# Optimization experiments

Measured on AMD Instinct MI355X. Metric: run time of the kernel, lower is better.

Reference implementation:

```python
import jax, jax.numpy as jnp
import numpy as np

B, S, D = 4, 4096, 1024

def setup_inputs() -> dict:
    key = jax.random.key(0)
    ks = jax.random.split(key, 7)
    scale = 1.0 / np.sqrt(D)
    X  = jax.random.normal(ks[0], (B, S, D), dtype=jnp.float32)
    Wq = jax.random.normal(ks[1], (D, D), dtype=jnp.float32) * scale
    bq = jnp.zeros((D,), dtype=jnp.float32)
    Wk = jax.random.normal(ks[2], (D, D), dtype=jnp.float32) * scale
    bk = jnp.zeros((D,), dtype=jnp.float32)
    Wv = jax.random.normal(ks[3], (D, D), dtype=jnp.float32) * scale
    bv = jnp.zeros((D,), dtype=jnp.float32)
    return {"X": X, "Wq": Wq, "bq": bq, "Wk": Wk, "bk": bk, "Wv": Wv, "bv": bv}

def reference(X, Wq, bq, Wk, bk, Wv, bv):
    # Linear projections (torch Linear: x @ W.T + b; here W stored as [D_in, D_out])
    Q = jnp.einsum('bsd,de->bse', X, Wq) + bq
    K = jnp.einsum('bsd,de->bse', X, Wk) + bk
    V = jnp.einsum('bsd,de->bse', X, Wv) + bv
    inv_sqrt_d = 1.0 / jnp.sqrt(jnp.float32(X.shape[-1]))
    scores = jnp.einsum('bqd,bkd->bqk', Q, K) * inv_sqrt_d  # [B,S,S]
    weights = jax.nn.sigmoid(scores)  # elementwise, no row normalization
    return jnp.einsum('bqk,bkd->bqd', weights, V)
```

## Files before the change

### kernel.cpp

```cpp
#include <hip/hip_runtime.h>
#include <hip/hip_bf16.h>

typedef __bf16 bf16_t;
typedef bf16_t bf16x8 __attribute__((ext_vector_type(8)));
typedef float f32x4 __attribute__((ext_vector_type(4)));

constexpr int BM = 128, BN = 128, BK = 32;
constexpr int D_DIM = 1024;
constexpr int S_DIM = 4096;
constexpr int B_DIM = 4;

__global__ void cast_f32_bf16(const float* __restrict__ in, bf16_t* __restrict__ out) {
  size_t i = ((size_t)blockIdx.x * blockDim.x + threadIdx.x) * 8;
  float4 a = *(const float4*)(in + i);
  float4 b = *(const float4*)(in + i + 4);
  bf16x8 o;
  o[0] = (bf16_t)a.x; o[1] = (bf16_t)a.y; o[2] = (bf16_t)a.z; o[3] = (bf16_t)a.w;
  o[4] = (bf16_t)b.x; o[5] = (bf16_t)b.y; o[6] = (bf16_t)b.z; o[7] = (bf16_t)b.w;
  *(bf16x8*)(out + i) = o;
}

__global__ void transpose_cast_1024(const float* __restrict__ in, bf16_t* __restrict__ out) {
  __shared__ float t[32][33];
  int x0 = blockIdx.x * 32, y0 = blockIdx.y * 32;
#pragma unroll
  for (int i = 0; i < 32; i += 8)
    t[threadIdx.y + i][threadIdx.x] =
        in[(size_t)(y0 + threadIdx.y + i) * D_DIM + (x0 + threadIdx.x)];
  __syncthreads();
#pragma unroll
  for (int i = 0; i < 32; i += 8)
    out[(size_t)(x0 + threadIdx.y + i) * D_DIM + (y0 + threadIdx.x)] =
        (bf16_t)t[threadIdx.x][threadIdx.y + i];
}

__device__ __forceinline__ void stage128x32(const bf16_t* __restrict__ g, int ld,
                                            bf16_t* lds, int tid) {
  int w = tid >> 6;
  int r = tid >> 2;
  int c = (tid & 3) * 8;
  const bf16_t* g0 = g + (size_t)r * ld + c;
  const bf16_t* g1 = g0 + (size_t)64 * ld;
  bf16_t* l0 = lds + w * 512;
  __builtin_amdgcn_global_load_lds((const __attribute__((address_space(1))) void*)g0,
                                   (__attribute__((address_space(3))) void*)l0, 16, 0, 0);
  __builtin_amdgcn_global_load_lds((const __attribute__((address_space(1))) void*)g1,
                                   (__attribute__((address_space(3))) void*)(l0 + 2048), 16, 0, 0);
}

template <int EPI, bool SWAP>
__global__ __launch_bounds__(256) void gemm_bt(
    const bf16_t* __restrict__ A, const bf16_t* __restrict__ Bt,
    void* __restrict__ C0, void* __restrict__ C1, void* __restrict__ C2,
    const float* __restrict__ b0, const float* __restrict__ b1, const float* __restrict__ b2,
    int K, int lda, int ldb, int ldc, float scale,
    size_t sA, size_t sB, size_t sC) {
  __shared__ bf16_t As[2 * BM * BK];
  __shared__ bf16_t Bs[2 * BN * BK];
  const int tid = threadIdx.x;
  const int lane = tid & 63;
  const int w = tid >> 6;
  const int wr = (w >> 1) * 64;
  const int wc = (w & 1) * 64;
  const int fm = lane & 15;
  const int fko = (lane >> 4) * 8;

  const int bx = SWAP ? blockIdx.y : blockIdx.x;
  const int by = SWAP ? blockIdx.x : blockIdx.y;

  const bf16_t* Ag = A + (size_t)blockIdx.z * sA + (size_t)by * BM * lda;
  const bf16_t* Bg = Bt + (size_t)blockIdx.z * sB + (size_t)bx * BN * ldb;

  f32x4 acc[4][4] = {};

  for (int k0 = 0; k0 < K; k0 += 2 * BK) {
    stage128x32(Ag + k0, lda, As, tid);
    stage128x32(Ag + k0 + BK, lda, As + BM * BK, tid);
    stage128x32(Bg + k0, ldb, Bs, tid);
    stage128x32(Bg + k0 + BK, ldb, Bs + BN * BK, tid);
    __syncthreads();
#pragma unroll
    for (int h = 0; h < 2; ++h) {
      const bf16_t* as = As + h * BM * BK;
      const bf16_t* bs = Bs + h * BN * BK;
      bf16x8 af[4], bfr[4];
#pragma unroll
      for (int i = 0; i < 4; ++i)
        af[i] = *(const bf16x8*)&as[(wr + i * 16 + fm) * BK + fko];
#pragma unroll
      for (int j = 0; j < 4; ++j)
        bfr[j] = *(const bf16x8*)&bs[(wc + j * 16 + fm) * BK + fko];
#pragma unroll
      for (int i = 0; i < 4; ++i)
#pragma unroll
        for (int j = 0; j < 4; ++j)
          acc[i][j] = __builtin_amdgcn_mfma_f32_16x16x32_bf16(af[i], bfr[j], acc[i][j], 0, 0, 0);
    }
    __syncthreads();
  }

  const int row0 = by * BM + wr + (lane >> 4) * 4;
  const int col0 = bx * BN + wc + fm;

  if constexpr (EPI == 0) {
    const int seg = (bx * BN) >> 10;
    const float* bias = (seg == 0) ? b0 : (seg == 1) ? b1 : b2;
#pragma unroll
    for (int i = 0; i < 4; ++i) {
#pragma unroll
      for (int j = 0; j < 4; ++j) {
        const int n = col0 + j * 16;
        const int nl = n & 1023;
        const float bv = bias[nl];
#pragma unroll
        for (int r = 0; r < 4; ++r) {
          const int m = row0 + i * 16 + r;
          float v = acc[i][j][r] + bv;
          if (seg < 2) {
            bf16_t* C = (bf16_t*)(seg == 0 ? C0 : C1);
            C[(size_t)m * D_DIM + nl] = (bf16_t)v;
          } else {
            bf16_t* C = (bf16_t*)C2;
            C[((size_t)(m >> 12) << 22) + (size_t)nl * S_DIM + (m & (S_DIM - 1))] = (bf16_t)v;
          }
        }
      }
    }
  } else {
#pragma unroll
    for (int i = 0; i < 4; ++i) {
#pragma unroll
      for (int j = 0; j < 4; ++j) {
        const int n = col0 + j * 16;
#pragma unroll
        for (int r = 0; r < 4; ++r) {
          const int m = row0 + i * 16 + r;
          float v = acc[i][j][r];
          if constexpr (EPI == 2) {
            bf16_t* C = (bf16_t*)C0 + (size_t)blockIdx.z * sC;
            float s = 1.0f / (1.0f + __expf(-v * scale));
            C[(size_t)m * ldc + n] = (bf16_t)s;
          } else {
            float* C = (float*)C0 + (size_t)blockIdx.z * sC;
            C[(size_t)m * ldc + n] = v;
          }
        }
      }
    }
  }
}

extern "C" void kernel_launch(void* const* d_in, const int* in_sizes, int n_in,
                              void* d_out, int out_size, void* d_ws, size_t ws_size,
                              hipStream_t stream) {
  const float* X  = (const float*)d_in[0];
  const float* Wq = (const float*)d_in[1];
  const float* bq = (const float*)d_in[2];
  const float* Wk = (const float*)d_in[3];
  const float* bk = (const float*)d_in[4];
  const float* Wv = (const float*)d_in[5];
  const float* bv = (const float*)d_in[6];
  float* out = (float*)d_out;

  const int M = B_DIM * S_DIM;
  const size_t SD = (size_t)S_DIM * D_DIM;
  const size_t E  = (size_t)M * D_DIM;
  const size_t PE1 = (size_t)S_DIM * S_DIM;
  const size_t WE = (size_t)D_DIM * D_DIM;

  size_t need4 = (4 * PE1 + 3 * E + 3 * WE) * sizeof(bf16_t);
  const int PB = (ws_size >= need4) ? 4 : 1;
  const size_t psz = (size_t)PB * PE1;

  bf16_t* ws = (bf16_t*)d_ws;
  bf16_t* P   = ws;
  bf16_t* Xb  = ws;
  bf16_t* Qb  = ws + psz;
  bf16_t* Kb  = Qb + E;
  bf16_t* Vt  = Kb + E;
  bf16_t* Wt  = Vt + E;

  cast_f32_bf16<<<dim3((unsigned)(E / 8 / 256)), dim3(256), 0, stream>>>(X, Xb);

  dim3 tg(D_DIM / 32, D_DIM / 32), tb(32, 8);
  transpose_cast_1024<<<tg, tb, 0, stream>>>(Wq, Wt);
  transpose_cast_1024<<<tg, tb, 0, stream>>>(Wk, Wt + WE);
  transpose_cast_1024<<<tg, tb, 0, stream>>>(Wv, Wt + 2 * WE);

  dim3 pg(3 * D_DIM / BN, M / BM, 1);
  gemm_bt<0, false><<<pg, 256, 0, stream>>>(Xb, Wt, Qb, Kb, Vt, bq, bk, bv,
                                            D_DIM, D_DIM, D_DIM, D_DIM, 1.0f, 0, 0, 0);

  const float scale = 0.03125f;
  for (int b0 = 0; b0 < B_DIM; b0 += PB) {
    dim3 sg(S_DIM / BN, S_DIM / BM, PB);
    gemm_bt<2, false><<<sg, 256, 0, stream>>>(Qb + (size_t)b0 * SD, Kb + (size_t)b0 * SD, P,
                                              nullptr, nullptr, nullptr, nullptr, nullptr,
                                              D_DIM, D_DIM, D_DIM, S_DIM, scale,
                                              SD, SD, PE1);
    dim3 vg(S_DIM / BM, D_DIM / BN, PB);
    gemm_bt<3, true><<<vg, 256, 0, stream>>>(P, Vt + (size_t)b0 * SD, out + (size_t)b0 * SD,
                                             nullptr, nullptr, nullptr, nullptr, nullptr,
                                             S_DIM, S_DIM, S_DIM, D_DIM, 1.0f,
                                             PE1, SD, SD);
  }
}
```

Measured before the change: 642.7 us.

## Replace GEMM with 256x256 tiled, swizzled, double-buffered 8-wave pipelined kernel

Replaces the 128x128 GEMM with a 256x256-tile kernel using 512 threads, a 128 KB LDS budget, and XOR-swizzled LDS layout to avoid bank conflicts. Global-to-LDS loads are interleaved with MFMA phases using explicit vmcnt waits, barriers and setprio, so memory traffic overlaps compute. The larger tile is meant to raise arithmetic intensity and hide load latency. In exchange it uses much more LDS per block, which limits occupancy, and the grid has fewer blocks, which could leave some compute units idle.

```diff
diff --git a/kernel.cpp b/kernel.cpp
--- a/kernel.cpp
+++ b/kernel.cpp
@@ -5,7 +5,6 @@
 typedef bf16_t bf16x8 __attribute__((ext_vector_type(8)));
 typedef float f32x4 __attribute__((ext_vector_type(4)));
 
-constexpr int BM = 128, BN = 128, BK = 32;
 constexpr int D_DIM = 1024;
 constexpr int S_DIM = 4096;
 constexpr int B_DIM = 4;
@@ -34,79 +33,171 @@
         (bf16_t)t[threadIdx.x][threadIdx.y + i];
 }
 
-__device__ __forceinline__ void stage128x32(const bf16_t* __restrict__ g, int ld,
-                                            bf16_t* lds, int tid) {
-  int w = tid >> 6;
-  int r = tid >> 2;
-  int c = (tid & 3) * 8;
-  const bf16_t* g0 = g + (size_t)r * ld + c;
-  const bf16_t* g1 = g0 + (size_t)64 * ld;
-  bf16_t* l0 = lds + w * 512;
-  __builtin_amdgcn_global_load_lds((const __attribute__((address_space(1))) void*)g0,
+constexpr int BM2 = 256, BN2 = 256;
+
+#define VMCNT4 asm volatile("s_waitcnt vmcnt(4)" ::: "memory")
+#define VMCNT0 asm volatile("s_waitcnt vmcnt(0)" ::: "memory")
+#define CFENCE asm volatile("" ::: "memory")
+#define BAR __builtin_amdgcn_s_barrier()
+#define PRIO1 __builtin_amdgcn_s_setprio(1)
+#define PRIO0 __builtin_amdgcn_s_setprio(0)
+
+__device__ __forceinline__ void stage_half(const bf16_t* __restrict__ g, int ld,
+                                           char* lds, int tid) {
+  const int w = tid >> 6, l = tid & 63;
+  const int rw = l >> 3;
+  const int gl = (l & 7) ^ rw;
+  char* l0 = lds + w * 1024;
+  const bf16_t* s0 = g + (size_t)(w * 8 + rw) * ld + gl * 8;
+  __builtin_amdgcn_global_load_lds((const __attribute__((address_space(1))) void*)s0,
                                    (__attribute__((address_space(3))) void*)l0, 16, 0, 0);
-  __builtin_amdgcn_global_load_lds((const __attribute__((address_space(1))) void*)g1,
-                                   (__attribute__((address_space(3))) void*)(l0 + 2048), 16, 0, 0);
+  __builtin_amdgcn_global_load_lds(
+      (const __attribute__((address_space(1))) void*)(s0 + (size_t)64 * ld),
+      (__attribute__((address_space(3))) void*)(l0 + 8192), 16, 0, 0);
+}
+
+__device__ __forceinline__ void load_a4(const char* __restrict__ At, int wr, int fm, int s,
+                                        int kxa, int kxb, bf16x8 (&af)[4][2]) {
+#pragma unroll
+  for (int m = 0; m < 4; ++m) {
+    const char* p = At + (wr + (s * 4 + m) * 16 + fm) * 128;
+    af[m][0] = *(const bf16x8*)(p + kxa);
+    af[m][1] = *(const bf16x8*)(p + kxb);
+  }
+}
+
+__device__ __forceinline__ void load_b8(const char* __restrict__ Bt_, int wc, int fm,
+                                        int kxa, int kxb, bf16x8 (&bfr)[4][2]) {
+#pragma unroll
+  for (int n = 0; n < 4; ++n) {
+    const char* p = Bt_ + (wc + n * 16 + fm) * 128;
+    bfr[n][0] = *(const bf16x8*)(p + kxa);
+    bfr[n][1] = *(const bf16x8*)(p + kxb);
+  }
+}
+
+__device__ __forceinline__ void mfma_q(f32x4 (&acc)[8][4], const bf16x8 (&af)[4][2],
+                                       const bf16x8 (&bfr)[4][2], int ms, int ns) {
+#pragma unroll
+  for (int m = 0; m < 4; ++m)
+#pragma unroll
+    for (int n = 0; n < 2; ++n)
+#pragma unroll
+      for (int kh = 0; kh < 2; ++kh)
+        acc[ms * 4 + m][ns * 2 + n] = __builtin_amdgcn_mfma_f32_16x16x32_bf16(
+            af[m][kh], bfr[ns * 2 + n][kh], acc[ms * 4 + m][ns * 2 + n], 0, 0, 0);
 }
 
 template <int EPI, bool SWAP>
-__global__ __launch_bounds__(256) void gemm_bt(
+__global__ __launch_bounds__(512, 2) void gemm256(
     const bf16_t* __restrict__ A, const bf16_t* __restrict__ Bt,
     void* __restrict__ C0, void* __restrict__ C1, void* __restrict__ C2,
     const float* __restrict__ b0, const float* __restrict__ b1, const float* __restrict__ b2,
     int K, int lda, int ldb, int ldc, float scale,
     size_t sA, size_t sB, size_t sC) {
-  __shared__ bf16_t As[2 * BM * BK];
-  __shared__ bf16_t Bs[2 * BN * BK];
+  __shared__ __align__(16) char smem[131072];
+  char* const A0t = smem;
+  char* const B0t = smem + 32768;
+  char* const A1t = smem + 65536;
+  char* const B1t = smem + 98304;
+
   const int tid = threadIdx.x;
   const int lane = tid & 63;
   const int w = tid >> 6;
-  const int wr = (w >> 1) * 64;
-  const int wc = (w & 1) * 64;
+  const int wr = (w >> 2) * 128;
+  const int wc = (w & 3) * 64;
   const int fm = lane & 15;
-  const int fko = (lane >> 4) * 8;
+  const int ssw = (fm & 7) << 4;
+  const int kp = (lane >> 4) << 4;
+  const int kxa = kp ^ ssw;
+  const int kxb = (64 | kp) ^ ssw;
 
   const int bx = SWAP ? blockIdx.y : blockIdx.x;
   const int by = SWAP ? blockIdx.x : blockIdx.y;
 
-  const bf16_t* Ag = A + (size_t)blockIdx.z * sA + (size_t)by * BM * lda;
-  const bf16_t* Bg = Bt + (size_t)blockIdx.z * sB + (size_t)bx * BN * ldb;
-
-  f32x4 acc[4][4] = {};
-
-  for (int k0 = 0; k0 < K; k0 += 2 * BK) {
-    stage128x32(Ag + k0, lda, As, tid);
-    stage128x32(Ag + k0 + BK, lda, As + BM * BK, tid);
-    stage128x32(Bg + k0, ldb, Bs, tid);
-    stage128x32(Bg + k0 + BK, ldb, Bs + BN * BK, tid);
-    __syncthreads();
-#pragma unroll
-    for (int h = 0; h < 2; ++h) {
-      const bf16_t* as = As + h * BM * BK;
-      const bf16_t* bs = Bs + h * BN * BK;
-      bf16x8 af[4], bfr[4];
-#pragma unroll
-      for (int i = 0; i < 4; ++i)
-        af[i] = *(const bf16x8*)&as[(wr + i * 16 + fm) * BK + fko];
-#pragma unroll
-      for (int j = 0; j < 4; ++j)
-        bfr[j] = *(const bf16x8*)&bs[(wc + j * 16 + fm) * BK + fko];
-#pragma unroll
-      for (int i = 0; i < 4; ++i)
-#pragma unroll
-        for (int j = 0; j < 4; ++j)
-          acc[i][j] = __builtin_amdgcn_mfma_f32_16x16x32_bf16(af[i], bfr[j], acc[i][j], 0, 0, 0);
-    }
-    __syncthreads();
-  }
-
-  const int row0 = by * BM + wr + (lane >> 4) * 4;
-  const int col0 = bx * BN + wc + fm;
+  const bf16_t* Ag = A + (size_t)blockIdx.z * sA + (size_t)by * BM2 * lda;
+  const bf16_t* Bg = Bt + (size_t)blockIdx.z * sB + (size_t)bx * BN2 * ldb;
+
+  f32x4 acc[8][4] = {};
+  bf16x8 af[4][2], bfr[4][2];
+
+  const int NI = K / 128;
+
+  stage_half(Ag, lda, A0t, tid);
+  stage_half(Ag + (size_t)128 * lda, lda, A0t + 16384, tid);
+  stage_half(Bg, ldb, B0t, tid);
+  stage_half(Bg + (size_t)128 * ldb, ldb, B0t + 16384, tid);
+  stage_half(Bg + 64, ldb, B1t, tid);
+  stage_half(Bg + 64 + (size_t)128 * ldb, ldb, B1t + 16384, tid);
+  VMCNT4;
+  BAR;
+
+  for (int it = 0; it < NI; ++it) {
+    const bool last = (it == NI - 1);
+    const bf16_t* Ao  = Ag + (size_t)(2 * it + 1) * 64;
+    const bf16_t* Ae2 = Ag + (size_t)(2 * it + 2) * 64;
+    const bf16_t* Be2 = Bg + (size_t)(2 * it + 2) * 64;
+    const bf16_t* Bo2 = Bg + (size_t)(2 * it + 3) * 64;
+
+    load_a4(A0t, wr, fm, 0, kxa, kxb, af);
+    load_b8(B0t, wc, fm, kxa, kxb, bfr);
+    stage_half(Ao, lda, A1t, tid);
+    CFENCE; BAR;
+    PRIO1; mfma_q(acc, af, bfr, 0, 0); PRIO0;
+    BAR;
+
+    load_a4(A0t, wr, fm, 1, kxa, kxb, af);
+    stage_half(Ao + (size_t)128 * lda, lda, A1t + 16384, tid);
+    if (!last) stage_half(Be2, ldb, B0t, tid);
+    CFENCE; BAR;
+    PRIO1; mfma_q(acc, af, bfr, 1, 0); PRIO0;
+    BAR;
+
+    if (!last) stage_half(Be2 + (size_t)128 * ldb, ldb, B0t + 16384, tid);
+    CFENCE; BAR;
+    PRIO1; mfma_q(acc, af, bfr, 1, 1); PRIO0;
+    BAR;
+
+    load_a4(A0t, wr, fm, 0, kxa, kxb, af);
+    CFENCE; BAR;
+    PRIO1; mfma_q(acc, af, bfr, 0, 1); PRIO0;
+    if (last) { VMCNT0; } else { VMCNT4; }
+    BAR;
+
+    load_a4(A1t, wr, fm, 0, kxa, kxb, af);
+    load_b8(B1t, wc, fm, kxa, kxb, bfr);
+    if (!last) stage_half(Ae2, lda, A0t, tid);
+    CFENCE; BAR;
+    PRIO1; mfma_q(acc, af, bfr, 0, 0); PRIO0;
+    BAR;
+
+    load_a4(A1t, wr, fm, 1, kxa, kxb, af);
+    if (!last) stage_half(Ae2 + (size_t)128 * lda, lda, A0t + 16384, tid);
+    CFENCE; BAR;
+    PRIO1; mfma_q(acc, af, bfr, 1, 0); PRIO0;
+    BAR;
+
+    if (!last) stage_half(Bo2, ldb, B1t, tid);
+    CFENCE; BAR;
+    PRIO1; mfma_q(acc, af, bfr, 1, 1); PRIO0;
+    BAR;
+
+    load_a4(A1t, wr, fm, 0, kxa, kxb, af);
+    if (!last) stage_half(Bo2 + (size_t)128 * ldb, ldb, B1t + 16384, tid);
+    CFENCE; BAR;
+    PRIO1; mfma_q(acc, af, bfr, 0, 1); PRIO0;
+    if (!last) { VMCNT4; }
+    BAR;
+  }
+
+  const int row0 = by * BM2 + wr + (lane >> 4) * 4;
+  const int col0 = bx * BN2 + wc + fm;
 
   if constexpr (EPI == 0) {
-    const int seg = (bx * BN) >> 10;
+    const int seg = bx >> 2;
     const float* bias = (seg == 0) ? b0 : (seg == 1) ? b1 : b2;
 #pragma unroll
-    for (int i = 0; i < 4; ++i) {
+    for (int i = 0; i < 8; ++i) {
 #pragma unroll
       for (int j = 0; j < 4; ++j) {
         const int n = col0 + j * 16;
@@ -128,7 +219,7 @@
     }
   } else {
 #pragma unroll
-    for (int i = 0; i < 4; ++i) {
+    for (int i = 0; i < 8; ++i) {
 #pragma unroll
       for (int j = 0; j < 4; ++j) {
         const int n = col0 + j * 16;
@@ -187,21 +278,21 @@
   transpose_cast_1024<<<tg, tb, 0, stream>>>(Wk, Wt + WE);
   transpose_cast_1024<<<tg, tb, 0, stream>>>(Wv, Wt + 2 * WE);
 
-  dim3 pg(3 * D_DIM / BN, M / BM, 1);
-  gemm_bt<0, false><<<pg, 256, 0, stream>>>(Xb, Wt, Qb, Kb, Vt, bq, bk, bv,
-                                            D_DIM, D_DIM, D_DIM, D_DIM, 1.0f, 0, 0, 0);
+  dim3 pg(3 * D_DIM / BN2, M / BM2, 1);
+  gemm256<0, false><<<pg, dim3(512), 0, stream>>>(
+      Xb, Wt, Qb, Kb, Vt, bq, bk, bv, D_DIM, D_DIM, D_DIM, D_DIM, 1.0f, 0, 0, 0);
 
   const float scale = 0.03125f;
   for (int b0 = 0; b0 < B_DIM; b0 += PB) {
-    dim3 sg(S_DIM / BN, S_DIM / BM, PB);
-    gemm_bt<2, false><<<sg, 256, 0, stream>>>(Qb + (size_t)b0 * SD, Kb + (size_t)b0 * SD, P,
-                                              nullptr, nullptr, nullptr, nullptr, nullptr,
-                                              D_DIM, D_DIM, D_DIM, S_DIM, scale,
-                                              SD, SD, PE1);
-    dim3 vg(S_DIM / BM, D_DIM / BN, PB);
-    gemm_bt<3, true><<<vg, 256, 0, stream>>>(P, Vt + (size_t)b0 * SD, out + (size_t)b0 * SD,
-                                             nullptr, nullptr, nullptr, nullptr, nullptr,
-                                             S_DIM, S_DIM, S_DIM, D_DIM, 1.0f,
-                                             PE1, SD, SD);
-  }
-}
+    dim3 sg(S_DIM / BN2, S_DIM / BM2, PB);
+    gemm256<2, false><<<sg, dim3(512), 0, stream>>>(
+        Qb + (size_t)b0 * SD, Kb + (size_t)b0 * SD, P,
+        nullptr, nullptr, nullptr, nullptr, nullptr,
+        D_DIM, D_DIM, D_DIM, S_DIM, scale, SD, SD, PE1);
+    dim3 vg(S_DIM / BM2, D_DIM / BN2, PB);
+    gemm256<3, true><<<vg, dim3(512), 0, stream>>>(
+        P, Vt + (size_t)b0 * SD, out + (size_t)b0 * SD,
+        nullptr, nullptr, nullptr, nullptr, nullptr,
+        S_DIM, S_DIM, S_DIM, D_DIM, 1.0f, PE1, SD, SD);
+  }
+}
```

Result: faster. 552.6 us (-14.0%).

## Replace GEMM with 256x256 tiles, 4-stage LDS pipeline and XCD-aware block remap

Applied to the files above, without the earlier changes.

Swaps the 128x128, 256-thread GEMM for a 256x256, 512-thread kernel. It keeps a four-deep ring of K=32 slices in LDS filled by global_load_lds, tuned with explicit vmcnt/lgkmcnt waits, barriers and priority bumps around the MFMA block. Workgroup indices are remapped in strides of eight so neighbouring tiles share a chiplet's L2. The goal is more operand reuse per tile and memory latency hidden behind MFMAs. The costs are higher register and LDS use (128 KB shared per block), fewer blocks in flight, and hand-coded wait counts that must match exactly.

```diff
diff --git a/kernel.cpp b/kernel.cpp
--- a/kernel.cpp
+++ b/kernel.cpp
@@ -5,7 +5,6 @@
 typedef bf16_t bf16x8 __attribute__((ext_vector_type(8)));
 typedef float f32x4 __attribute__((ext_vector_type(4)));
 
-constexpr int BM = 128, BN = 128, BK = 32;
 constexpr int D_DIM = 1024;
 constexpr int S_DIM = 4096;
 constexpr int B_DIM = 4;
@@ -34,79 +33,123 @@
         (bf16_t)t[threadIdx.x][threadIdx.y + i];
 }
 
-__device__ __forceinline__ void stage128x32(const bf16_t* __restrict__ g, int ld,
-                                            bf16_t* lds, int tid) {
-  int w = tid >> 6;
-  int r = tid >> 2;
-  int c = (tid & 3) * 8;
-  const bf16_t* g0 = g + (size_t)r * ld + c;
-  const bf16_t* g1 = g0 + (size_t)64 * ld;
+constexpr int BM2 = 256, BN2 = 256;
+
+#define VMCNT8 asm volatile("s_waitcnt vmcnt(8)" ::: "memory")
+#define VMCNT4 asm volatile("s_waitcnt vmcnt(4)" ::: "memory")
+#define VMCNT0 asm volatile("s_waitcnt vmcnt(0)" ::: "memory")
+#define LGKM8  asm volatile("s_waitcnt lgkmcnt(8)" ::: "memory")
+#define LGKM0  asm volatile("s_waitcnt lgkmcnt(0)" ::: "memory")
+#define SCHEDB __builtin_amdgcn_sched_barrier(0)
+#define CFENCE asm volatile("" ::: "memory")
+#define BAR __builtin_amdgcn_s_barrier()
+#define PRIO1 __builtin_amdgcn_s_setprio(1)
+#define PRIO0 __builtin_amdgcn_s_setprio(0)
+
+__device__ __forceinline__ void stage_tile32(const bf16_t* __restrict__ g, int ld,
+                                             bf16_t* lds, int tid) {
+  const int w = tid >> 6, l = tid & 63;
+  const int row = w * 16 + (l >> 2);
+  const int chunk = (l & 3) * 8;
+  const bf16_t* s0 = g + (size_t)row * ld + chunk;
   bf16_t* l0 = lds + w * 512;
-  __builtin_amdgcn_global_load_lds((const __attribute__((address_space(1))) void*)g0,
+  __builtin_amdgcn_global_load_lds((const __attribute__((address_space(1))) void*)s0,
                                    (__attribute__((address_space(3))) void*)l0, 16, 0, 0);
-  __builtin_amdgcn_global_load_lds((const __attribute__((address_space(1))) void*)g1,
-                                   (__attribute__((address_space(3))) void*)(l0 + 2048), 16, 0, 0);
+  __builtin_amdgcn_global_load_lds(
+      (const __attribute__((address_space(1))) void*)(s0 + (size_t)128 * ld),
+      (__attribute__((address_space(3))) void*)(l0 + 4096), 16, 0, 0);
 }
 
 template <int EPI, bool SWAP>
-__global__ __launch_bounds__(256) void gemm_bt(
+__global__ __launch_bounds__(512, 2) void gemm256k32(
     const bf16_t* __restrict__ A, const bf16_t* __restrict__ Bt,
     void* __restrict__ C0, void* __restrict__ C1, void* __restrict__ C2,
     const float* __restrict__ b0, const float* __restrict__ b1, const float* __restrict__ b2,
     int K, int lda, int ldb, int ldc, float scale,
     size_t sA, size_t sB, size_t sC) {
-  __shared__ bf16_t As[2 * BM * BK];
-  __shared__ bf16_t Bs[2 * BN * BK];
+  __shared__ __align__(16) bf16_t smem[65536];
+
   const int tid = threadIdx.x;
   const int lane = tid & 63;
   const int w = tid >> 6;
-  const int wr = (w >> 1) * 64;
-  const int wc = (w & 1) * 64;
+  const int wr = (w >> 2) * 128;
+  const int wc = (w & 3) * 64;
   const int fm = lane & 15;
   const int fko = (lane >> 4) * 8;
 
-  const int bx = SWAP ? blockIdx.y : blockIdx.x;
-  const int by = SWAP ? blockIdx.x : blockIdx.y;
-
-  const bf16_t* Ag = A + (size_t)blockIdx.z * sA + (size_t)by * BM * lda;
-  const bf16_t* Bg = Bt + (size_t)blockIdx.z * sB + (size_t)bx * BN * ldb;
-
-  f32x4 acc[4][4] = {};
-
-  for (int k0 = 0; k0 < K; k0 += 2 * BK) {
-    stage128x32(Ag + k0, lda, As, tid);
-    stage128x32(Ag + k0 + BK, lda, As + BM * BK, tid);
-    stage128x32(Bg + k0, ldb, Bs, tid);
-    stage128x32(Bg + k0 + BK, ldb, Bs + BN * BK, tid);
-    __syncthreads();
-#pragma unroll
-    for (int h = 0; h < 2; ++h) {
-      const bf16_t* as = As + h * BM * BK;
-      const bf16_t* bs = Bs + h * BN * BK;
-      bf16x8 af[4], bfr[4];
-#pragma unroll
-      for (int i = 0; i < 4; ++i)
-        af[i] = *(const bf16x8*)&as[(wr + i * 16 + fm) * BK + fko];
-#pragma unroll
-      for (int j = 0; j < 4; ++j)
-        bfr[j] = *(const bf16x8*)&bs[(wc + j * 16 + fm) * BK + fko];
-#pragma unroll
-      for (int i = 0; i < 4; ++i)
-#pragma unroll
-        for (int j = 0; j < 4; ++j)
-          acc[i][j] = __builtin_amdgcn_mfma_f32_16x16x32_bf16(af[i], bfr[j], acc[i][j], 0, 0, 0);
+  const int nx = gridDim.x, ny = gridDim.y;
+  const int nwg = nx * ny * gridDim.z;
+  const int flat = blockIdx.x + nx * (blockIdx.y + ny * blockIdx.z);
+  const int q = nwg >> 3;
+  const int L = (flat & 7) * q + (flat >> 3);
+  const int lx = L % nx;
+  const int lt = L / nx;
+  const int ly = lt % ny;
+  const int lz = lt / ny;
+
+  const int bx = SWAP ? ly : lx;
+  const int by = SWAP ? lx : ly;
+
+  const bf16_t* Ag = A + (size_t)lz * sA + (size_t)by * BM2 * lda;
+  const bf16_t* Bg = Bt + (size_t)lz * sB + (size_t)bx * BN2 * ldb;
+
+  f32x4 acc[8][4] = {};
+  bf16x8 af[8], bfr[4];
+
+  const int NT = K / 32;
+
+  stage_tile32(Ag, lda, smem, tid);
+  stage_tile32(Bg, ldb, smem + 8192, tid);
+  stage_tile32(Ag + 32, lda, smem + 16384, tid);
+  stage_tile32(Bg + 32, ldb, smem + 16384 + 8192, tid);
+  stage_tile32(Ag + 64, lda, smem + 32768, tid);
+  stage_tile32(Bg + 64, ldb, smem + 32768 + 8192, tid);
+  VMCNT8;
+  BAR;
+
+#pragma unroll 1
+  for (int t = 0; t < NT; ++t) {
+    const bf16_t* As = smem + (t & 3) * 16384;
+    const bf16_t* Bs = As + 8192;
+
+#pragma unroll
+    for (int m = 0; m < 8; ++m)
+      af[m] = *(const bf16x8*)&As[(wr + m * 16 + fm) * 32 + fko];
+#pragma unroll
+    for (int n = 0; n < 4; ++n)
+      bfr[n] = *(const bf16x8*)&Bs[(wc + n * 16 + fm) * 32 + fko];
+
+    if (t + 3 < NT) {
+      bf16_t* dst = smem + ((t + 3) & 3) * 16384;
+      stage_tile32(Ag + (size_t)(t + 3) * 32, lda, dst, tid);
+      stage_tile32(Bg + (size_t)(t + 3) * 32, ldb, dst + 8192, tid);
     }
-    __syncthreads();
+
+    LGKM8; CFENCE; BAR;
+    LGKM0; SCHEDB;
+    PRIO1;
+#pragma unroll
+    for (int m = 0; m < 8; ++m)
+#pragma unroll
+      for (int n = 0; n < 4; ++n)
+        acc[m][n] = __builtin_amdgcn_mfma_f32_16x16x32_bf16(af[m], bfr[n], acc[m][n], 0, 0, 0);
+    PRIO0;
+
+    const int rem = NT - 1 - t;
+    if (rem >= 3) { VMCNT8; }
+    else if (rem == 2) { VMCNT4; }
+    else if (rem == 1) { VMCNT0; }
+    BAR;
   }
 
-  const int row0 = by * BM + wr + (lane >> 4) * 4;
-  const int col0 = bx * BN + wc + fm;
+  const int row0 = by * BM2 + wr + (lane >> 4) * 4;
+  const int col0 = bx * BN2 + wc + fm;
 
   if constexpr (EPI == 0) {
-    const int seg = (bx * BN) >> 10;
+    const int seg = bx >> 2;
     const float* bias = (seg == 0) ? b0 : (seg == 1) ? b1 : b2;
 #pragma unroll
-    for (int i = 0; i < 4; ++i) {
+    for (int i = 0; i < 8; ++i) {
 #pragma unroll
       for (int j = 0; j < 4; ++j) {
         const int n = col0 + j * 16;
@@ -128,7 +171,7 @@
     }
   } else {
 #pragma unroll
-    for (int i = 0; i < 4; ++i) {
+    for (int i = 0; i < 8; ++i) {
 #pragma unroll
       for (int j = 0; j < 4; ++j) {
         const int n = col0 + j * 16;
@@ -137,11 +180,11 @@
           const int m = row0 + i * 16 + r;
           float v = acc[i][j][r];
           if constexpr (EPI == 2) {
-            bf16_t* C = (bf16_t*)C0 + (size_t)blockIdx.z * sC;
+            bf16_t* C = (bf16_t*)C0 + (size_t)lz * sC;
             float s = 1.0f / (1.0f + __expf(-v * scale));
             C[(size_t)m * ldc + n] = (bf16_t)s;
           } else {
-            float* C = (float*)C0 + (size_t)blockIdx.z * sC;
+            float* C = (float*)C0 + (size_t)lz * sC;
             C[(size_t)m * ldc + n] = v;
           }
         }
@@ -187,21 +230,21 @@
   transpose_cast_1024<<<tg, tb, 0, stream>>>(Wk, Wt + WE);
   transpose_cast_1024<<<tg, tb, 0, stream>>>(Wv, Wt + 2 * WE);
 
-  dim3 pg(3 * D_DIM / BN, M / BM, 1);
-  gemm_bt<0, false><<<pg, 256, 0, stream>>>(Xb, Wt, Qb, Kb, Vt, bq, bk, bv,
-                                            D_DIM, D_DIM, D_DIM, D_DIM, 1.0f, 0, 0, 0);
+  dim3 pg(3 * D_DIM / BN2, M / BM2, 1);
+  gemm256k32<0, false><<<pg, dim3(512), 0, stream>>>(
+      Xb, Wt, Qb, Kb, Vt, bq, bk, bv, D_DIM, D_DIM, D_DIM, D_DIM, 1.0f, 0, 0, 0);
 
   const float scale = 0.03125f;
   for (int b0 = 0; b0 < B_DIM; b0 += PB) {
-    dim3 sg(S_DIM / BN, S_DIM / BM, PB);
-    gemm_bt<2, false><<<sg, 256, 0, stream>>>(Qb + (size_t)b0 * SD, Kb + (size_t)b0 * SD, P,
-                                              nullptr, nullptr, nullptr, nullptr, nullptr,
-                                              D_DIM, D_DIM, D_DIM, S_DIM, scale,
-                                              SD, SD, PE1);
-    dim3 vg(S_DIM / BM, D_DIM / BN, PB);
-    gemm_bt<3, true><<<vg, 256, 0, stream>>>(P, Vt + (size_t)b0 * SD, out + (size_t)b0 * SD,
-                                             nullptr, nullptr, nullptr, nullptr, nullptr,
-                                             S_DIM, S_DIM, S_DIM, D_DIM, 1.0f,
-                                             PE1, SD, SD);
+    dim3 sg(S_DIM / BN2, S_DIM / BM2, PB);
+    gemm256k32<2, false><<<sg, dim3(512), 0, stream>>>(
+        Qb + (size_t)b0 * SD, Kb + (size_t)b0 * SD, P,
+        nullptr, nullptr, nullptr, nullptr, nullptr,
+        D_DIM, D_DIM, D_DIM, S_DIM, scale, SD, SD, PE1);
+    dim3 vg(S_DIM / BM2, D_DIM / BN2, PB);
+    gemm256k32<3, true><<<vg, dim3(512), 0, stream>>>(
+        P, Vt + (size_t)b0 * SD, out + (size_t)b0 * SD,
+        nullptr, nullptr, nullptr, nullptr, nullptr,
+        S_DIM, S_DIM, S_DIM, D_DIM, 1.0f, PE1, SD, SD);
   }
 }
```

New measurement: 604.2 us. 6.0% less time.
